# Kernel tuning notes

Measured on AMD Instinct MI355X. Metric: run time of the kernel, lower is better.

The kernel has to match this reference:

```python
import jax, jax.numpy as jnp
import numpy as np

B, N = 512, 4
OBS, OBSU, ID = 128, 64, 16
STATE = OBS + OBSU - ID  # 176
M1, M2, G1, A = 256, 256, 256, 16
E = 128  # hypernet_embed


def setup_inputs() -> dict:
    key = jax.random.key(0)
    ks = jax.random.split(key, 24)

    def W(k, shape):
        return jax.random.normal(k, shape, dtype=jnp.float32) * 0.05

    inp = {"input": jax.random.normal(ks[0], (B, N, OBS + OBSU), dtype=jnp.float32)}
    # layer1_hypernet: Linear(ID, 10*E)
    inp["l1_W"] = W(ks[1], (10 * E, ID)); inp["l1_b"] = W(ks[2], (10 * E,))
    # hyper_net{i}_w / hyper_net{i}_b : Linear(E, in*out) / Linear(E, out)
    inp["w1W"] = W(ks[3], (STATE * M1, E)); inp["w1b"] = W(ks[4], (STATE * M1,))
    inp["b1W"] = W(ks[5], (M1, E));        inp["b1b"] = W(ks[6], (M1,))
    inp["w2W"] = W(ks[7], (M1 * M2, E));   inp["w2b"] = W(ks[8], (M1 * M2,))
    inp["b2W"] = W(ks[9], (M2, E));        inp["b2b"] = W(ks[10], (M2,))
    inp["w3W"] = W(ks[11], (M2 * M2, E));  inp["w3b"] = W(ks[12], (M2 * M2,))
    inp["b3W"] = W(ks[13], (M2, E));       inp["b3b"] = W(ks[14], (M2,))
    inp["w4W"] = W(ks[15], (M2 * G1, E));  inp["w4b"] = W(ks[16], (M2 * G1,))
    inp["b4W"] = W(ks[17], (G1, E));       inp["b4b"] = W(ks[18], (G1,))
    inp["w5W"] = W(ks[19], (G1 * A, E));   inp["w5b"] = W(ks[20], (G1 * A,))
    inp["b5W"] = W(ks[21], (A, E));        inp["b5b"] = W(ks[22], (A,))
    return inp


def reference(input, l1_W, l1_b, w1W, w1b, b1W, b1b, w2W, w2b, b2W, b2b,
              w3W, w3b, b3W, b3b, w4W, w4b, b4W, b4b, w5W, w5b, b5W, b5b):
    b, n, d = input.shape
    BN = b * n
    ids = input[..., -ID:].reshape(BN, ID)
    x = input[..., :-ID].reshape(BN, d - ID)  # [BN, STATE]
    # layer1_hypernet: ReLU(Linear(ID -> 10E))
    h = jax.nn.relu(ids @ l1_W.T + l1_b)  # [BN, 10E]
    chunk = lambda i: h[:, i * E:(i + 1) * E]

    def layer(x, iw, ib, wW, wb, bW, bb, out_dim, act):
        # generate per-sample weight [BN, in, out] and bias [BN, out]
        Wm = (chunk(iw) @ wW.T + wb).reshape(BN, x.shape[-1], out_dim)
        bm = chunk(ib) @ bW.T + bb
        y = jnp.einsum('bs,bsm->bm', x, Wm) + bm  # batched GEMV
        return jax.nn.relu(y) if act else y

    out = layer(x,   0, 1, w1W, w1b, b1W, b1b, M1, True)
    out = layer(out, 2, 3, w2W, w2b, b2W, b2b, M2, True)
    out = layer(out, 4, 5, w3W, w3b, b3W, b3b, M2, True)
    out = layer(out, 6, 7, w4W, w4b, b4W, b4b, G1, False)  # no ReLU after layer 4
    out = layer(out, 8, 9, w5W, w5b, b5W, b5b, A, True)
    return out.reshape(b, n, A)
```

## Files before the change

kernel.cpp:

```cpp
#include <hip/hip_runtime.h>
#include <hip/hip_bf16.h>

#define E_ 128
#define NSAMP 2048

typedef __attribute__((ext_vector_type(8))) short short8;
typedef __attribute__((ext_vector_type(4))) float floatx4;

__device__ __forceinline__ ushort f2b(float f) {
    union { __hip_bfloat16 h; ushort u; } cv;
    cv.h = __float2bfloat16(f);
    return cv.u;
}

__device__ __forceinline__ void gload_lds16(const ushort* g, ushort* l) {
    __builtin_amdgcn_global_load_lds(
        (const __attribute__((address_space(1))) void*)g,
        (__attribute__((address_space(3))) void*)l, 16, 0, 0);
}

__global__ void hyper_h(const float* __restrict__ input, const float* __restrict__ l1W,
                        const float* __restrict__ l1b, float* __restrict__ h)
{
    int b = blockIdx.x / 5;
    int o = (blockIdx.x % 5) * 256 + threadIdx.x;
    const float* ids = input + (size_t)b * 192 + 176;
    const float* w = l1W + (size_t)o * 16;
    float a = l1b[o];
#pragma unroll
    for (int i = 0; i < 16; i += 4) {
        float4 wv = *(const float4*)(w + i);
        a += ids[i] * wv.x + ids[i + 1] * wv.y + ids[i + 2] * wv.z + ids[i + 3] * wv.w;
    }
    h[(size_t)b * 1280 + o] = fmaxf(a, 0.f);
}

__global__ void x0_t(const float* __restrict__ input, float* __restrict__ xT0)
{
    int idx = blockIdx.x * 256 + threadIdx.x;
    int s = idx >> 11, b = idx & 2047;
    xT0[idx] = input[(size_t)b * 192 + s];
}

__global__ void cvt_bf16(const float* __restrict__ src, ushort* __restrict__ dst, int n)
{
    int i = (blockIdx.x * 256 + threadIdx.x) * 8;
    if (i >= n) return;
    float4 a = *(const float4*)(src + i);
    float4 b = *(const float4*)(src + i + 4);
    union { ushort o[8]; uint4 v; } u;
    u.o[0] = f2b(a.x); u.o[1] = f2b(a.y); u.o[2] = f2b(a.z); u.o[3] = f2b(a.w);
    u.o[4] = f2b(b.x); u.o[5] = f2b(b.y); u.o[6] = f2b(b.z); u.o[7] = f2b(b.w);
    *(uint4*)(dst + i) = u.v;
}

__global__ void cvt_bias(const float* __restrict__ bW, const float* __restrict__ wb,
                         ushort* __restrict__ dst, int S, int M)
{
    int idx = blockIdx.x * 256 + threadIdx.x;
    int slice = idx / (M * E_);
    int rem = idx - slice * (M * E_);
    int m = rem / E_, e = rem - m * E_;
    ushort v;
    if (slice == 0) {
        v = f2b(bW[(size_t)m * E_ + e]);
    } else {
        int s = (slice - 1) * 128 + e;
        v = (s < S) ? f2b(wb[(size_t)s * M + m]) : (ushort)0;
    }
    dst[(size_t)(S + slice) * M * E_ + rem] = v;
}

__global__ __launch_bounds__(256, 2) void gemm_big(
    const ushort* __restrict__ wWb, const float* __restrict__ h,
    const float* __restrict__ xT, float* __restrict__ partial,
    int S, int iw, int ksplit, int btiles, int ntiles)
{
    __shared__ ushort As[128 * 64];
    __shared__ ushort Bs[128 * 64];

    const int tid = threadIdx.x;
    const int bt = blockIdx.x % btiles;
    const int nt = (blockIdx.x / btiles) % ntiles;
    const int ks = blockIdx.x / (btiles * ntiles);
    const int b0 = bt * 128;
    const int m0 = nt * 128;
    const int total_s = S + 3;
    const int base = total_s / ksplit;
    const int rem = total_s - base * ksplit;
    const int s0 = ks * base + min(ks, rem);
    const int s1 = s0 + base + (ks < rem ? 1 : 0);

    const int lane = tid & 63;
    const int wave = tid >> 6;
    const int quad = lane >> 4;
    const int lr = lane & 15;
    const int wm0 = (wave >> 1) * 64;
    const int wn0 = (wave & 1) * 64;

    const int tb = tid >> 3;
    const int teg = tid & 7;
    const int aswz = (teg ^ (tb & 7)) * 8;

    const int brow = lane >> 3;
    const int bgg = (lane & 7) ^ brow;

    float hreg[4][2][8];
#pragma unroll
    for (int k2 = 0; k2 < 4; ++k2) {
#pragma unroll
        for (int p = 0; p < 2; ++p) {
            const float* src = h + (size_t)(b0 + tb + 32 * k2) * 1280 + (size_t)iw * E_ + p * 64 + teg * 8;
            float4 v0 = *(const float4*)(src);
            float4 v1 = *(const float4*)(src + 4);
            hreg[k2][p][0] = v0.x; hreg[k2][p][1] = v0.y; hreg[k2][p][2] = v0.z; hreg[k2][p][3] = v0.w;
            hreg[k2][p][4] = v1.x; hreg[k2][p][5] = v1.y; hreg[k2][p][6] = v1.z; hreg[k2][p][7] = v1.w;
        }
    }

    floatx4 acc[4][4];
#pragma unroll
    for (int i = 0; i < 4; ++i)
#pragma unroll
        for (int j = 0; j < 4; ++j)
            acc[i][j] = (floatx4){0.f, 0.f, 0.f, 0.f};

    for (int s = s0; s < s1; ++s) {
        float xv[4];
        if (s < S) {
#pragma unroll
            for (int k2 = 0; k2 < 4; ++k2)
                xv[k2] = xT[(size_t)s * NSAMP + b0 + tb + 32 * k2];
        }

#pragma unroll
        for (int p = 0; p < 2; ++p) {
            __syncthreads();

#pragma unroll
            for (int t = 0; t < 4; ++t) {
                int rloc = wave * 32 + t * 8;
                const ushort* gp = wWb + ((size_t)s * 256 + m0 + rloc + brow) * E_ + p * 64 + bgg * 8;
                ushort* lp = &Bs[(size_t)rloc * 64] + lane * 8;
                gload_lds16(gp, lp);
            }

            if (s < S) {
#pragma unroll
                for (int k2 = 0; k2 < 4; ++k2) {
                    union { ushort o[8]; uint4 v; } u;
#pragma unroll
                    for (int j = 0; j < 8; ++j) u.o[j] = f2b(xv[k2] * hreg[k2][p][j]);
                    *(uint4*)&As[(size_t)(tb + 32 * k2) * 64 + aswz] = u.v;
                }
            } else if (s == S) {
#pragma unroll
                for (int k2 = 0; k2 < 4; ++k2) {
                    const float* src = h + (size_t)(b0 + tb + 32 * k2) * 1280
                                         + (size_t)(iw + 1) * E_ + p * 64 + teg * 8;
                    float4 v0 = *(const float4*)(src);
                    float4 v1 = *(const float4*)(src + 4);
                    union { ushort o[8]; uint4 v; } u;
                    u.o[0] = f2b(v0.x); u.o[1] = f2b(v0.y); u.o[2] = f2b(v0.z); u.o[3] = f2b(v0.w);
                    u.o[4] = f2b(v1.x); u.o[5] = f2b(v1.y); u.o[6] = f2b(v1.z); u.o[7] = f2b(v1.w);
                    *(uint4*)&As[(size_t)(tb + 32 * k2) * 64 + aswz] = u.v;
                }
            } else {
                int j0 = (s - S - 1) * 128 + p * 64 + teg * 8;
#pragma unroll
                for (int k2 = 0; k2 < 4; ++k2) {
                    int b = b0 + tb + 32 * k2;
                    union { ushort o[8]; uint4 v; } u;
#pragma unroll
                    for (int jj = 0; jj < 8; ++jj) {
                        int sp = j0 + jj;
                        u.o[jj] = (sp < S) ? f2b(xT[(size_t)sp * NSAMP + b]) : (ushort)0;
                    }
                    *(uint4*)&As[(size_t)(tb + 32 * k2) * 64 + aswz] = u.v;
                }
            }

            __syncthreads();

#pragma unroll
            for (int kk = 0; kk < 2; ++kk) {
                const int swz = ((kk * 4 + quad) ^ (lr & 7)) * 8;
                short8 af[4], bfr[4];
#pragma unroll
                for (int i = 0; i < 4; ++i)
                    af[i] = *(const short8*)&As[(size_t)(wm0 + i * 16 + lr) * 64 + swz];
#pragma unroll
                for (int j = 0; j < 4; ++j)
                    bfr[j] = *(const short8*)&Bs[(size_t)(wn0 + j * 16 + lr) * 64 + swz];
#pragma unroll
                for (int i = 0; i < 4; ++i)
#pragma unroll
                    for (int j = 0; j < 4; ++j)
                        acc[i][j] = __builtin_amdgcn_mfma_f32_16x16x32_bf16(af[i], bfr[j], acc[i][j], 0, 0, 0);
            }
        }
    }

    float* dst = partial + (size_t)ks * NSAMP * 256;
#pragma unroll
    for (int i = 0; i < 4; ++i)
#pragma unroll
        for (int j = 0; j < 4; ++j)
#pragma unroll
            for (int r = 0; r < 4; ++r) {
                int row = wm0 + i * 16 + quad * 4 + r;
                int col = wn0 + j * 16 + lr;
                dst[(size_t)(b0 + row) * 256 + m0 + col] = acc[i][j][r];
            }
}

template<int BM, int BN, int WROWS, int WCOLS>
__global__ __launch_bounds__(256, 2) void gemm_k(
    const ushort* __restrict__ wWb, const float* __restrict__ h,
    const float* __restrict__ xT, float* __restrict__ partial,
    int S, int M, int iw, int ksplit, int btiles, int ntiles)
{
    constexpr int SM = BM / WROWS / 16;
    constexpr int SN = BN / WCOLS / 16;
    constexpr int ASLOTS = BM * 8 / 256;
    constexpr int LDA = 72;

    __shared__ ushort As[BM][LDA];
    __shared__ ushort Bs[BN][LDA];

    const int tid = threadIdx.x;
    const int bt = blockIdx.x % btiles;
    const int nt = (blockIdx.x / btiles) % ntiles;
    const int ks = blockIdx.x / (btiles * ntiles);
    const int b0 = bt * BM;
    const int m0 = nt * BN;
    const int total_s = S + 3;
    const int base = total_s / ksplit;
    const int rem = total_s - base * ksplit;
    const int s0 = ks * base + min(ks, rem);
    const int s1 = s0 + base + (ks < rem ? 1 : 0);

    const int lane = tid & 63;
    const int wave = tid >> 6;
    const int quad = lane >> 4;
    const int lr = lane & 15;
    const int wm0 = (wave / WCOLS) * (BM / WROWS);
    const int wn0 = (wave % WCOLS) * (BN / WCOLS);

    const int tb = tid >> 3;
    const int teg = tid & 7;

    float hreg[ASLOTS][2][8];
#pragma unroll
    for (int k2 = 0; k2 < ASLOTS; ++k2) {
        int b = tb + 32 * k2;
#pragma unroll
        for (int p = 0; p < 2; ++p) {
            const float* src = h + (size_t)(b0 + b) * 1280 + (size_t)iw * E_ + p * 64 + teg * 8;
            float4 v0 = *(const float4*)(src);
            float4 v1 = *(const float4*)(src + 4);
            hreg[k2][p][0] = v0.x; hreg[k2][p][1] = v0.y; hreg[k2][p][2] = v0.z; hreg[k2][p][3] = v0.w;
            hreg[k2][p][4] = v1.x; hreg[k2][p][5] = v1.y; hreg[k2][p][6] = v1.z; hreg[k2][p][7] = v1.w;
        }
    }

    floatx4 acc[SM][SN];
#pragma unroll
    for (int i = 0; i < SM; ++i)
#pragma unroll
        for (int j = 0; j < SN; ++j)
            acc[i][j] = (floatx4){0.f, 0.f, 0.f, 0.f};

    for (int s = s0; s < s1; ++s) {
        float xv[ASLOTS];
        if (s < S) {
#pragma unroll
            for (int k2 = 0; k2 < ASLOTS; ++k2)
                xv[k2] = xT[(size_t)s * NSAMP + b0 + tb + 32 * k2];
        }

#pragma unroll
        for (int p = 0; p < 2; ++p) {
            if (s < S) {
#pragma unroll
                for (int k2 = 0; k2 < ASLOTS; ++k2) {
                    union { ushort o[8]; uint4 v; } u;
#pragma unroll
                    for (int j = 0; j < 8; ++j) u.o[j] = f2b(xv[k2] * hreg[k2][p][j]);
                    *(uint4*)&As[tb + 32 * k2][teg * 8] = u.v;
                }
            } else if (s == S) {
#pragma unroll
                for (int k2 = 0; k2 < ASLOTS; ++k2) {
                    const float* src = h + (size_t)(b0 + tb + 32 * k2) * 1280
                                         + (size_t)(iw + 1) * E_ + p * 64 + teg * 8;
                    float4 v0 = *(const float4*)(src);
                    float4 v1 = *(const float4*)(src + 4);
                    union { ushort o[8]; uint4 v; } u;
                    u.o[0] = f2b(v0.x); u.o[1] = f2b(v0.y); u.o[2] = f2b(v0.z); u.o[3] = f2b(v0.w);
                    u.o[4] = f2b(v1.x); u.o[5] = f2b(v1.y); u.o[6] = f2b(v1.z); u.o[7] = f2b(v1.w);
                    *(uint4*)&As[tb + 32 * k2][teg * 8] = u.v;
                }
            } else {
                int j0 = (s - S - 1) * 128 + p * 64 + teg * 8;
#pragma unroll
                for (int k2 = 0; k2 < ASLOTS; ++k2) {
                    int b = b0 + tb + 32 * k2;
                    union { ushort o[8]; uint4 v; } u;
#pragma unroll
                    for (int jj = 0; jj < 8; ++jj) {
                        int sp = j0 + jj;
                        u.o[jj] = (sp < S) ? f2b(xT[(size_t)sp * NSAMP + b]) : (ushort)0;
                    }
                    *(uint4*)&As[tb + 32 * k2][teg * 8] = u.v;
                }
            }
#pragma unroll
            for (int slot = tid; slot < BN * 8; slot += 256) {
                int m = slot >> 3, eg2 = slot & 7;
                *(uint4*)&Bs[m][eg2 * 8] =
                    *(const uint4*)(wWb + ((size_t)s * M + m0 + m) * E_ + p * 64 + eg2 * 8);
            }
            __syncthreads();
#pragma unroll
            for (int kk = 0; kk < 2; ++kk) {
                short8 af[SM], bfr[SN];
#pragma unroll
                for (int i = 0; i < SM; ++i)
                    af[i] = *(const short8*)&As[wm0 + i * 16 + lr][kk * 32 + quad * 8];
#pragma unroll
                for (int j = 0; j < SN; ++j)
                    bfr[j] = *(const short8*)&Bs[wn0 + j * 16 + lr][kk * 32 + quad * 8];
#pragma unroll
                for (int i = 0; i < SM; ++i)
#pragma unroll
                    for (int j = 0; j < SN; ++j)
                        acc[i][j] = __builtin_amdgcn_mfma_f32_16x16x32_bf16(af[i], bfr[j], acc[i][j], 0, 0, 0);
            }
            __syncthreads();
        }
    }

    float* dst = partial + (size_t)ks * NSAMP * M;
#pragma unroll
    for (int i = 0; i < SM; ++i)
#pragma unroll
        for (int j = 0; j < SN; ++j)
#pragma unroll
            for (int r = 0; r < 4; ++r) {
                int row = wm0 + i * 16 + quad * 4 + r;
                int col = wn0 + j * 16 + lr;
                dst[(size_t)(b0 + row) * M + m0 + col] = acc[i][j][r];
            }
}

__global__ void reduce_mid(const float* __restrict__ partial, const float* __restrict__ bb,
                           float* __restrict__ xTn, int KS, int relu)
{
    __shared__ float t[32][33];
    const int b0 = (blockIdx.x >> 3) * 32;
    const int m0 = (blockIdx.x & 7) * 32;
    const int mo = threadIdx.x & 31;
    const int bs0 = threadIdx.x >> 5;
    const float bv = bb[m0 + mo];
#pragma unroll
    for (int r = 0; r < 4; ++r) {
        const int bs = bs0 + 8 * r;
        const size_t off = (size_t)(b0 + bs) * 256 + m0 + mo;
        float a0 = 0.f, a1 = 0.f, a2 = 0.f, a3 = 0.f;
#pragma unroll
        for (int k = 0; k < 16; k += 4) {
            a0 += partial[(size_t)(k + 0) * (NSAMP * 256) + off];
            a1 += partial[(size_t)(k + 1) * (NSAMP * 256) + off];
            a2 += partial[(size_t)(k + 2) * (NSAMP * 256) + off];
            a3 += partial[(size_t)(k + 3) * (NSAMP * 256) + off];
        }
        float a = (a0 + a1) + (a2 + a3) + bv;
        if (relu) a = fmaxf(a, 0.f);
        t[bs][mo] = a;
    }
    __syncthreads();
    const int bo = threadIdx.x & 31;
    const int ms0 = threadIdx.x >> 5;
#pragma unroll
    for (int r = 0; r < 4; ++r) {
        const int ms = ms0 + 8 * r;
        xTn[(size_t)(m0 + ms) * NSAMP + b0 + bo] = t[bo][ms];
    }
}

__global__ void reduce_out(const float* __restrict__ partial, const float* __restrict__ bb,
                           float* __restrict__ out, int KS)
{
    int idx = blockIdx.x * 256 + threadIdx.x;
    float a0 = 0.f, a1 = 0.f, a2 = 0.f, a3 = 0.f;
#pragma unroll
    for (int k = 0; k < 32; k += 4) {
        a0 += partial[(size_t)(k + 0) * (NSAMP * 16) + idx];
        a1 += partial[(size_t)(k + 1) * (NSAMP * 16) + idx];
        a2 += partial[(size_t)(k + 2) * (NSAMP * 16) + idx];
        a3 += partial[(size_t)(k + 3) * (NSAMP * 16) + idx];
    }
    out[idx] = fmaxf((a0 + a1) + (a2 + a3) + bb[idx & 15], 0.f);
}

extern "C" void kernel_launch(void* const* d_in, const int* in_sizes, int n_in,
                              void* d_out, int out_size, void* d_ws, size_t ws_size,
                              hipStream_t stream)
{
    const float* input = (const float*)d_in[0];
    const float* l1W   = (const float*)d_in[1];
    const float* l1b   = (const float*)d_in[2];

    char* ws = (char*)d_ws;
    ushort* wWb = (ushort*)(ws + 0);
    float* h    = (float*)(ws + 16975872);
    float* xT0  = (float*)(ws + 27461632);
    float* xT1  = (float*)(ws + 29558784);
    float* part = (float*)(ws + 31655936);

    hipLaunchKernelGGL(hyper_h, dim3(2048 * 5), dim3(256), 0, stream, input, l1W, l1b, h);
    hipLaunchKernelGGL(x0_t, dim3(176 * 2048 / 256), dim3(256), 0, stream, input, xT0);

    const int S_[5] = {176, 256, 256, 256, 256};
    const int M_[5] = {256, 256, 256, 256, 16};
    float* xt[2] = {xT0, xT1};

    for (int i = 0; i < 5; ++i) {
        const float* wW = (const float*)d_in[3 + 4 * i];
        const float* wb = (const float*)d_in[4 + 4 * i];
        const float* bW = (const float*)d_in[5 + 4 * i];
        const float* bb = (const float*)d_in[6 + 4 * i];
        float* xin = xt[i & 1];
        int n = S_[i] * M_[i] * E_;
        hipLaunchKernelGGL(cvt_bf16, dim3(n / 2048), dim3(256), 0, stream, wW, wWb, n);
        hipLaunchKernelGGL(cvt_bias, dim3(3 * M_[i] * E_ / 256), dim3(256), 0, stream,
                           bW, wb, wWb, S_[i], M_[i]);

        if (M_[i] == 256) {
            const int btiles = 16, ntiles = 2, ksplit = 16;
            hipLaunchKernelGGL(gemm_big, dim3(btiles * ntiles * ksplit), dim3(256), 0, stream,
                               wWb, h, xin, part, S_[i], 2 * i, ksplit, btiles, ntiles);
            hipLaunchKernelGGL(reduce_mid, dim3(512), dim3(256), 0, stream,
                               part, bb, xt[(i + 1) & 1], ksplit, (i < 3) ? 1 : 0);
        } else {
            const int btiles = 8, ntiles = 1, ksplit = 32;
            hipLaunchKernelGGL((gemm_k<256, 16, 4, 1>), dim3(btiles * ntiles * ksplit), dim3(256), 0, stream,
                               wWb, h, xin, part, S_[i], 16, 2 * i, ksplit, btiles, ntiles);
            hipLaunchKernelGGL(reduce_out, dim3(128), dim3(256), 0, stream,
                               part, bb, (float*)d_out, ksplit);
        }
    }
}
```

Baseline: 580.3 us.

## Double-buffer LDS tiles in gemm_big to overlap weight DMA with MFMA

Splits the A and B shared-memory tiles into two buffers and restructures the loop into a software pipeline. The next phase's weight tile is DMA'd into the alternate buffer and its A tile generated there while the current phase's MFMAs run, cutting the two barriers per phase to one. This doubles LDS use to 64 KB per block, which may limit the two-blocks-per-CU occupancy target and raise register pressure.

```diff
diff --git a/kernel.cpp b/kernel.cpp
--- a/kernel.cpp
+++ b/kernel.cpp
@@ -76,8 +76,8 @@
     const float* __restrict__ xT, float* __restrict__ partial,
     int S, int iw, int ksplit, int btiles, int ntiles)
 {
-    __shared__ ushort As[128 * 64];
-    __shared__ ushort Bs[128 * 64];
+    __shared__ ushort As[2][128 * 64];
+    __shared__ ushort Bs[2][128 * 64];
 
     const int tid = threadIdx.x;
     const int bt = blockIdx.x % btiles;
@@ -125,79 +125,106 @@
         for (int j = 0; j < 4; ++j)
             acc[i][j] = (floatx4){0.f, 0.f, 0.f, 0.f};
 
-    for (int s = s0; s < s1; ++s) {
-        float xv[4];
+    float xv[4];
+
+    auto dma_B = [&](int s, int p, int buf) {
+#pragma unroll
+        for (int t = 0; t < 4; ++t) {
+            int rloc = wave * 32 + t * 8;
+            const ushort* gp = wWb + ((size_t)s * 256 + m0 + rloc + brow) * E_ + p * 64 + bgg * 8;
+            gload_lds16(gp, &Bs[buf][rloc * 64 + lane * 8]);
+        }
+    };
+
+    auto gen_A = [&](int s, int p, int buf) {
         if (s < S) {
 #pragma unroll
+            for (int k2 = 0; k2 < 4; ++k2) {
+                union { ushort o[8]; uint4 v; } u;
+#pragma unroll
+                for (int j = 0; j < 8; ++j) u.o[j] = f2b(xv[k2] * hreg[k2][p][j]);
+                *(uint4*)&As[buf][(tb + 32 * k2) * 64 + aswz] = u.v;
+            }
+        } else if (s == S) {
+#pragma unroll
+            for (int k2 = 0; k2 < 4; ++k2) {
+                const float* src = h + (size_t)(b0 + tb + 32 * k2) * 1280
+                                     + (size_t)(iw + 1) * E_ + p * 64 + teg * 8;
+                float4 v0 = *(const float4*)(src);
+                float4 v1 = *(const float4*)(src + 4);
+                union { ushort o[8]; uint4 v; } u;
+                u.o[0] = f2b(v0.x); u.o[1] = f2b(v0.y); u.o[2] = f2b(v0.z); u.o[3] = f2b(v0.w);
+                u.o[4] = f2b(v1.x); u.o[5] = f2b(v1.y); u.o[6] = f2b(v1.z); u.o[7] = f2b(v1.w);
+                *(uint4*)&As[buf][(tb + 32 * k2) * 64 + aswz] = u.v;
+            }
+        } else {
+            int j0 = (s - S - 1) * 128 + p * 64 + teg * 8;
+#pragma unroll
+            for (int k2 = 0; k2 < 4; ++k2) {
+                int b = b0 + tb + 32 * k2;
+                union { ushort o[8]; uint4 v; } u;
+#pragma unroll
+                for (int jj = 0; jj < 8; ++jj) {
+                    int sp = j0 + jj;
+                    u.o[jj] = (sp < S) ? f2b(xT[(size_t)sp * NSAMP + b]) : (ushort)0;
+                }
+                *(uint4*)&As[buf][(tb + 32 * k2) * 64 + aswz] = u.v;
+            }
+        }
+    };
+
+    const int nph = (s1 - s0) * 2;
+
+    if (s0 < S) {
+#pragma unroll
+        for (int k2 = 0; k2 < 4; ++k2)
+            xv[k2] = xT[(size_t)s0 * NSAMP + b0 + tb + 32 * k2];
+    }
+    dma_B(s0, 0, 0);
+    gen_A(s0, 0, 0);
+
+    for (int ph = 0; ph < nph; ++ph) {
+        const int cur = ph & 1;
+        const int np = ph + 1;
+        const int sn = s0 + (np >> 1);
+        const int pn = np & 1;
+        const bool stage = np < nph;
+
+        __syncthreads();
+
+        if (stage) dma_B(sn, pn, cur ^ 1);
+
+        float xvn[4];
+        const bool newx = stage && pn == 0 && sn < S;
+        if (newx) {
+#pragma unroll
             for (int k2 = 0; k2 < 4; ++k2)
-                xv[k2] = xT[(size_t)s * NSAMP + b0 + tb + 32 * k2];
-        }
-
-#pragma unroll
-        for (int p = 0; p < 2; ++p) {
-            __syncthreads();
-
-#pragma unroll
-            for (int t = 0; t < 4; ++t) {
-                int rloc = wave * 32 + t * 8;
-                const ushort* gp = wWb + ((size_t)s * 256 + m0 + rloc + brow) * E_ + p * 64 + bgg * 8;
-                ushort* lp = &Bs[(size_t)rloc * 64] + lane * 8;
-                gload_lds16(gp, lp);
-            }
-
-            if (s < S) {
-#pragma unroll
-                for (int k2 = 0; k2 < 4; ++k2) {
-                    union { ushort o[8]; uint4 v; } u;
-#pragma unroll
-                    for (int j = 0; j < 8; ++j) u.o[j] = f2b(xv[k2] * hreg[k2][p][j]);
-                    *(uint4*)&As[(size_t)(tb + 32 * k2) * 64 + aswz] = u.v;
-                }
-            } else if (s == S) {
-#pragma unroll
-                for (int k2 = 0; k2 < 4; ++k2) {
-                    const float* src = h + (size_t)(b0 + tb + 32 * k2) * 1280
-                                         + (size_t)(iw + 1) * E_ + p * 64 + teg * 8;
-                    float4 v0 = *(const float4*)(src);
-                    float4 v1 = *(const float4*)(src + 4);
-                    union { ushort o[8]; uint4 v; } u;
-                    u.o[0] = f2b(v0.x); u.o[1] = f2b(v0.y); u.o[2] = f2b(v0.z); u.o[3] = f2b(v0.w);
-                    u.o[4] = f2b(v1.x); u.o[5] = f2b(v1.y); u.o[6] = f2b(v1.z); u.o[7] = f2b(v1.w);
-                    *(uint4*)&As[(size_t)(tb + 32 * k2) * 64 + aswz] = u.v;
-                }
-            } else {
-                int j0 = (s - S - 1) * 128 + p * 64 + teg * 8;
-#pragma unroll
-                for (int k2 = 0; k2 < 4; ++k2) {
-                    int b = b0 + tb + 32 * k2;
-                    union { ushort o[8]; uint4 v; } u;
-#pragma unroll
-                    for (int jj = 0; jj < 8; ++jj) {
-                        int sp = j0 + jj;
-                        u.o[jj] = (sp < S) ? f2b(xT[(size_t)sp * NSAMP + b]) : (ushort)0;
-                    }
-                    *(uint4*)&As[(size_t)(tb + 32 * k2) * 64 + aswz] = u.v;
-                }
-            }
-
-            __syncthreads();
-
-#pragma unroll
-            for (int kk = 0; kk < 2; ++kk) {
-                const int swz = ((kk * 4 + quad) ^ (lr & 7)) * 8;
-                short8 af[4], bfr[4];
-#pragma unroll
-                for (int i = 0; i < 4; ++i)
-                    af[i] = *(const short8*)&As[(size_t)(wm0 + i * 16 + lr) * 64 + swz];
+                xvn[k2] = xT[(size_t)sn * NSAMP + b0 + tb + 32 * k2];
+        }
+
+#pragma unroll
+        for (int kk = 0; kk < 2; ++kk) {
+            const int swz = ((kk * 4 + quad) ^ (lr & 7)) * 8;
+            short8 af[4], bfr[4];
+#pragma unroll
+            for (int i = 0; i < 4; ++i)
+                af[i] = *(const short8*)&As[cur][(wm0 + i * 16 + lr) * 64 + swz];
+#pragma unroll
+            for (int j = 0; j < 4; ++j)
+                bfr[j] = *(const short8*)&Bs[cur][(wn0 + j * 16 + lr) * 64 + swz];
+#pragma unroll
+            for (int i = 0; i < 4; ++i)
 #pragma unroll
                 for (int j = 0; j < 4; ++j)
-                    bfr[j] = *(const short8*)&Bs[(size_t)(wn0 + j * 16 + lr) * 64 + swz];
-#pragma unroll
-                for (int i = 0; i < 4; ++i)
-#pragma unroll
-                    for (int j = 0; j < 4; ++j)
-                        acc[i][j] = __builtin_amdgcn_mfma_f32_16x16x32_bf16(af[i], bfr[j], acc[i][j], 0, 0, 0);
-            }
+                    acc[i][j] = __builtin_amdgcn_mfma_f32_16x16x32_bf16(af[i], bfr[j], acc[i][j], 0, 0, 0);
+        }
+
+        if (stage) {
+            if (newx) {
+#pragma unroll
+                for (int k2 = 0; k2 < 4; ++k2) xv[k2] = xvn[k2];
+            }
+            gen_A(sn, pn, cur ^ 1);
         }
     }
 
```

New measurement: 791.0 us. 36.3% more time.

## Restructure hypernet GEMM to factor x out of per-s MFMA and double-buffer weights

Applied to the files above, without the earlier changes.

The large-layer GEMM no longer builds an x*h product tile in LDS for each state index. It keeps bf16 h fragments in registers, computes W_s·h per s with MFMA, and scales the result by x[s] in fp32 before accumulating. Full 128x128 weight slices are double-buffered in LDS so the next slice loads while the current one is computed. The partial-output layout is transposed to [m][b], which lets reduce_mid become a plain vectorized sum with no LDS transpose. The risk is extra fp32 FMA work per s, higher register pressure, and more LDS use (64KB) that may lower occupancy.

```diff
diff --git a/kernel.cpp b/kernel.cpp
--- a/kernel.cpp
+++ b/kernel.cpp
@@ -71,50 +71,57 @@
     dst[(size_t)(S + slice) * M * E_ + rem] = v;
 }
 
-__global__ __launch_bounds__(256, 2) void gemm_big(
+__global__ __launch_bounds__(256, 2) void gemm_big2(
     const ushort* __restrict__ wWb, const float* __restrict__ h,
     const float* __restrict__ xT, float* __restrict__ partial,
-    int S, int iw, int ksplit, int btiles, int ntiles)
-{
-    __shared__ ushort As[128 * 64];
-    __shared__ ushort Bs[128 * 64];
+    int S, int iw, int ksplit)
+{
+    __shared__ ushort Ws[2][128 * 128];
 
     const int tid = threadIdx.x;
-    const int bt = blockIdx.x % btiles;
-    const int nt = (blockIdx.x / btiles) % ntiles;
-    const int ks = blockIdx.x / (btiles * ntiles);
+    const int mt = blockIdx.x & 1;
+    const int bt = (blockIdx.x >> 1) & 15;
+    const int ks = blockIdx.x >> 5;
+    const int m0 = mt * 128;
     const int b0 = bt * 128;
-    const int m0 = nt * 128;
     const int total_s = S + 3;
     const int base = total_s / ksplit;
     const int rem = total_s - base * ksplit;
     const int s0 = ks * base + min(ks, rem);
     const int s1 = s0 + base + (ks < rem ? 1 : 0);
+    const int sm = min(s1, S);
 
     const int lane = tid & 63;
     const int wave = tid >> 6;
     const int quad = lane >> 4;
     const int lr = lane & 15;
-    const int wm0 = (wave >> 1) * 64;
-    const int wn0 = (wave & 1) * 64;
-
-    const int tb = tid >> 3;
-    const int teg = tid & 7;
-    const int aswz = (teg ^ (tb & 7)) * 8;
-
-    const int brow = lane >> 3;
-    const int bgg = (lane & 7) ^ brow;
-
-    float hreg[4][2][8];
-#pragma unroll
-    for (int k2 = 0; k2 < 4; ++k2) {
-#pragma unroll
-        for (int p = 0; p < 2; ++p) {
-            const float* src = h + (size_t)(b0 + tb + 32 * k2) * 1280 + (size_t)iw * E_ + p * 64 + teg * 8;
-            float4 v0 = *(const float4*)(src);
-            float4 v1 = *(const float4*)(src + 4);
-            hreg[k2][p][0] = v0.x; hreg[k2][p][1] = v0.y; hreg[k2][p][2] = v0.z; hreg[k2][p][3] = v0.w;
-            hreg[k2][p][4] = v1.x; hreg[k2][p][5] = v1.y; hreg[k2][p][6] = v1.z; hreg[k2][p][7] = v1.w;
+    const int wm = (wave >> 1) * 64;
+    const int wb_ = (wave & 1) * 64;
+
+    const int dr = lane >> 4;
+    const int dg = lane & 15;
+
+#pragma unroll
+    for (int t = 0; t < 8; ++t) {
+        int rbase = (wave * 8 + t) * 4;
+        int r = rbase + dr;
+        int g = (dg & 8) | ((dg & 7) ^ (r & 7));
+        gload_lds16(wWb + ((size_t)s0 * 256 + m0 + r) * 128 + g * 8,
+                    &Ws[0][rbase * 128 + lane * 8]);
+    }
+
+    short8 hf[4][4];
+#pragma unroll
+    for (int j = 0; j < 4; ++j) {
+        const float* hr = h + (size_t)(b0 + wb_ + j * 16 + lr) * 1280 + (size_t)iw * E_;
+#pragma unroll
+        for (int kk = 0; kk < 4; ++kk) {
+            float4 v0 = *(const float4*)(hr + kk * 32 + quad * 8);
+            float4 v1 = *(const float4*)(hr + kk * 32 + quad * 8 + 4);
+            union { ushort o[8]; short8 v; } u;
+            u.o[0] = f2b(v0.x); u.o[1] = f2b(v0.y); u.o[2] = f2b(v0.z); u.o[3] = f2b(v0.w);
+            u.o[4] = f2b(v1.x); u.o[5] = f2b(v1.y); u.o[6] = f2b(v1.z); u.o[7] = f2b(v1.w);
+            hf[j][kk] = u.v;
         }
     }
 
@@ -125,92 +132,132 @@
         for (int j = 0; j < 4; ++j)
             acc[i][j] = (floatx4){0.f, 0.f, 0.f, 0.f};
 
-    for (int s = s0; s < s1; ++s) {
+    const floatx4 zf = (floatx4){0.f, 0.f, 0.f, 0.f};
+
+    int cur = 0;
+    for (int s = s0; s < sm; ++s) {
         float xv[4];
-        if (s < S) {
-#pragma unroll
-            for (int k2 = 0; k2 < 4; ++k2)
-                xv[k2] = xT[(size_t)s * NSAMP + b0 + tb + 32 * k2];
-        }
-
-#pragma unroll
-        for (int p = 0; p < 2; ++p) {
-            __syncthreads();
-
-#pragma unroll
-            for (int t = 0; t < 4; ++t) {
-                int rloc = wave * 32 + t * 8;
-                const ushort* gp = wWb + ((size_t)s * 256 + m0 + rloc + brow) * E_ + p * 64 + bgg * 8;
-                ushort* lp = &Bs[(size_t)rloc * 64] + lane * 8;
-                gload_lds16(gp, lp);
-            }
-
-            if (s < S) {
-#pragma unroll
-                for (int k2 = 0; k2 < 4; ++k2) {
-                    union { ushort o[8]; uint4 v; } u;
-#pragma unroll
-                    for (int j = 0; j < 8; ++j) u.o[j] = f2b(xv[k2] * hreg[k2][p][j]);
-                    *(uint4*)&As[(size_t)(tb + 32 * k2) * 64 + aswz] = u.v;
-                }
-            } else if (s == S) {
-#pragma unroll
-                for (int k2 = 0; k2 < 4; ++k2) {
-                    const float* src = h + (size_t)(b0 + tb + 32 * k2) * 1280
-                                         + (size_t)(iw + 1) * E_ + p * 64 + teg * 8;
-                    float4 v0 = *(const float4*)(src);
-                    float4 v1 = *(const float4*)(src + 4);
-                    union { ushort o[8]; uint4 v; } u;
+#pragma unroll
+        for (int j = 0; j < 4; ++j)
+            xv[j] = xT[(size_t)s * NSAMP + b0 + wb_ + j * 16 + lr];
+
+        __syncthreads();
+
+        if (s + 1 < sm) {
+#pragma unroll
+            for (int t = 0; t < 8; ++t) {
+                int rbase = (wave * 8 + t) * 4;
+                int r = rbase + dr;
+                int g = (dg & 8) | ((dg & 7) ^ (r & 7));
+                gload_lds16(wWb + ((size_t)(s + 1) * 256 + m0 + r) * 128 + g * 8,
+                            &Ws[cur ^ 1][rbase * 128 + lane * 8]);
+            }
+        }
+
+#pragma unroll
+        for (int i = 0; i < 4; ++i) {
+            const int r = wm + i * 16 + lr;
+            short8 af[4];
+#pragma unroll
+            for (int kk = 0; kk < 4; ++kk) {
+                int g = kk * 4 + quad;
+                int g2 = (g & 8) | ((g & 7) ^ (r & 7));
+                af[kk] = *(const short8*)&Ws[cur][r * 128 + g2 * 8];
+            }
+            floatx4 Gj[4];
+#pragma unroll
+            for (int j = 0; j < 4; ++j)
+                Gj[j] = __builtin_amdgcn_mfma_f32_16x16x32_bf16(af[0], hf[j][0], zf, 0, 0, 0);
+#pragma unroll
+            for (int kk = 1; kk < 4; ++kk)
+#pragma unroll
+                for (int j = 0; j < 4; ++j)
+                    Gj[j] = __builtin_amdgcn_mfma_f32_16x16x32_bf16(af[kk], hf[j][kk], Gj[j], 0, 0, 0);
+#pragma unroll
+            for (int j = 0; j < 4; ++j)
+                acc[i][j] += xv[j] * Gj[j];
+        }
+        cur ^= 1;
+    }
+
+    for (int s = sm; s < s1; ++s) {
+        __syncthreads();
+#pragma unroll
+        for (int t = 0; t < 8; ++t) {
+            int rbase = (wave * 8 + t) * 4;
+            int r = rbase + dr;
+            int g = (dg & 8) | ((dg & 7) ^ (r & 7));
+            gload_lds16(wWb + ((size_t)s * 256 + m0 + r) * 128 + g * 8,
+                        &Ws[0][rbase * 128 + lane * 8]);
+        }
+        short8 bfb[4][4];
+        if (s == S) {
+#pragma unroll
+            for (int j = 0; j < 4; ++j) {
+                const float* hr = h + (size_t)(b0 + wb_ + j * 16 + lr) * 1280 + (size_t)(iw + 1) * E_;
+#pragma unroll
+                for (int kk = 0; kk < 4; ++kk) {
+                    float4 v0 = *(const float4*)(hr + kk * 32 + quad * 8);
+                    float4 v1 = *(const float4*)(hr + kk * 32 + quad * 8 + 4);
+                    union { ushort o[8]; short8 v; } u;
                     u.o[0] = f2b(v0.x); u.o[1] = f2b(v0.y); u.o[2] = f2b(v0.z); u.o[3] = f2b(v0.w);
                     u.o[4] = f2b(v1.x); u.o[5] = f2b(v1.y); u.o[6] = f2b(v1.z); u.o[7] = f2b(v1.w);
-                    *(uint4*)&As[(size_t)(tb + 32 * k2) * 64 + aswz] = u.v;
+                    bfb[j][kk] = u.v;
                 }
-            } else {
-                int j0 = (s - S - 1) * 128 + p * 64 + teg * 8;
-#pragma unroll
-                for (int k2 = 0; k2 < 4; ++k2) {
-                    int b = b0 + tb + 32 * k2;
-                    union { ushort o[8]; uint4 v; } u;
-#pragma unroll
-                    for (int jj = 0; jj < 8; ++jj) {
-                        int sp = j0 + jj;
-                        u.o[jj] = (sp < S) ? f2b(xT[(size_t)sp * NSAMP + b]) : (ushort)0;
+            }
+        } else {
+            int off = (s - S - 1) * 128;
+#pragma unroll
+            for (int j = 0; j < 4; ++j) {
+                int b = b0 + wb_ + j * 16 + lr;
+#pragma unroll
+                for (int kk = 0; kk < 4; ++kk) {
+                    union { ushort o[8]; short8 v; } u;
+#pragma unroll
+                    for (int t = 0; t < 8; ++t) {
+                        int sp = off + kk * 32 + quad * 8 + t;
+                        u.o[t] = (sp < S) ? f2b(xT[(size_t)sp * NSAMP + b]) : (ushort)0;
                     }
-                    *(uint4*)&As[(size_t)(tb + 32 * k2) * 64 + aswz] = u.v;
+                    bfb[j][kk] = u.v;
                 }
             }
-
-            __syncthreads();
-
-#pragma unroll
-            for (int kk = 0; kk < 2; ++kk) {
-                const int swz = ((kk * 4 + quad) ^ (lr & 7)) * 8;
-                short8 af[4], bfr[4];
-#pragma unroll
-                for (int i = 0; i < 4; ++i)
-                    af[i] = *(const short8*)&As[(size_t)(wm0 + i * 16 + lr) * 64 + swz];
+        }
+        __syncthreads();
+#pragma unroll
+        for (int i = 0; i < 4; ++i) {
+            const int r = wm + i * 16 + lr;
+            short8 af[4];
+#pragma unroll
+            for (int kk = 0; kk < 4; ++kk) {
+                int g = kk * 4 + quad;
+                int g2 = (g & 8) | ((g & 7) ^ (r & 7));
+                af[kk] = *(const short8*)&Ws[0][r * 128 + g2 * 8];
+            }
+            floatx4 Gj[4];
+#pragma unroll
+            for (int j = 0; j < 4; ++j)
+                Gj[j] = __builtin_amdgcn_mfma_f32_16x16x32_bf16(af[0], bfb[j][0], zf, 0, 0, 0);
+#pragma unroll
+            for (int kk = 1; kk < 4; ++kk)
 #pragma unroll
                 for (int j = 0; j < 4; ++j)
-                    bfr[j] = *(const short8*)&Bs[(size_t)(wn0 + j * 16 + lr) * 64 + swz];
-#pragma unroll
-                for (int i = 0; i < 4; ++i)
-#pragma unroll
-                    for (int j = 0; j < 4; ++j)
-                        acc[i][j] = __builtin_amdgcn_mfma_f32_16x16x32_bf16(af[i], bfr[j], acc[i][j], 0, 0, 0);
-            }
-        }
-    }
-
-    float* dst = partial + (size_t)ks * NSAMP * 256;
+                    Gj[j] = __builtin_amdgcn_mfma_f32_16x16x32_bf16(af[kk], bfb[j][kk], Gj[j], 0, 0, 0);
+#pragma unroll
+            for (int j = 0; j < 4; ++j)
+                acc[i][j] += Gj[j];
+        }
+    }
+
+    float* dst = partial + (size_t)ks * (256 * NSAMP);
 #pragma unroll
     for (int i = 0; i < 4; ++i)
 #pragma unroll
         for (int j = 0; j < 4; ++j)
 #pragma unroll
             for (int r = 0; r < 4; ++r) {
-                int row = wm0 + i * 16 + quad * 4 + r;
-                int col = wn0 + j * 16 + lr;
-                dst[(size_t)(b0 + row) * 256 + m0 + col] = acc[i][j][r];
+                int m = m0 + wm + i * 16 + quad * 4 + r;
+                int b = b0 + wb_ + j * 16 + lr;
+                dst[(size_t)m * NSAMP + b] = acc[i][j][r];
             }
 }
 
@@ -357,36 +404,22 @@
 __global__ void reduce_mid(const float* __restrict__ partial, const float* __restrict__ bb,
                            float* __restrict__ xTn, int KS, int relu)
 {
-    __shared__ float t[32][33];
-    const int b0 = (blockIdx.x >> 3) * 32;
-    const int m0 = (blockIdx.x & 7) * 32;
-    const int mo = threadIdx.x & 31;
-    const int bs0 = threadIdx.x >> 5;
-    const float bv = bb[m0 + mo];
-#pragma unroll
-    for (int r = 0; r < 4; ++r) {
-        const int bs = bs0 + 8 * r;
-        const size_t off = (size_t)(b0 + bs) * 256 + m0 + mo;
-        float a0 = 0.f, a1 = 0.f, a2 = 0.f, a3 = 0.f;
-#pragma unroll
-        for (int k = 0; k < 16; k += 4) {
-            a0 += partial[(size_t)(k + 0) * (NSAMP * 256) + off];
-            a1 += partial[(size_t)(k + 1) * (NSAMP * 256) + off];
-            a2 += partial[(size_t)(k + 2) * (NSAMP * 256) + off];
-            a3 += partial[(size_t)(k + 3) * (NSAMP * 256) + off];
-        }
-        float a = (a0 + a1) + (a2 + a3) + bv;
-        if (relu) a = fmaxf(a, 0.f);
-        t[bs][mo] = a;
-    }
-    __syncthreads();
-    const int bo = threadIdx.x & 31;
-    const int ms0 = threadIdx.x >> 5;
-#pragma unroll
-    for (int r = 0; r < 4; ++r) {
-        const int ms = ms0 + 8 * r;
-        xTn[(size_t)(m0 + ms) * NSAMP + b0 + bo] = t[bo][ms];
-    }
+    int idx = (blockIdx.x * 256 + threadIdx.x) * 4;
+    int m = idx >> 11;
+    floatx4 a0 = {0.f,0.f,0.f,0.f}, a1 = a0, a2 = a0, a3 = a0;
+#pragma unroll 4
+    for (int k = 0; k < KS; k += 4) {
+        a0 += *(const floatx4*)&partial[(size_t)(k + 0) * (256 * NSAMP) + idx];
+        a1 += *(const floatx4*)&partial[(size_t)(k + 1) * (256 * NSAMP) + idx];
+        a2 += *(const floatx4*)&partial[(size_t)(k + 2) * (256 * NSAMP) + idx];
+        a3 += *(const floatx4*)&partial[(size_t)(k + 3) * (256 * NSAMP) + idx];
+    }
+    floatx4 r = (a0 + a1) + (a2 + a3) + bb[m];
+    if (relu) {
+        r[0] = fmaxf(r[0], 0.f); r[1] = fmaxf(r[1], 0.f);
+        r[2] = fmaxf(r[2], 0.f); r[3] = fmaxf(r[3], 0.f);
+    }
+    *(floatx4*)&xTn[idx] = r;
 }
 
 __global__ void reduce_out(const float* __restrict__ partial, const float* __restrict__ bb,
@@ -438,11 +471,10 @@
                            bW, wb, wWb, S_[i], M_[i]);
 
         if (M_[i] == 256) {
-            const int btiles = 16, ntiles = 2, ksplit = 16;
-            hipLaunchKernelGGL(gemm_big, dim3(btiles * ntiles * ksplit), dim3(256), 0, stream,
-                               wWb, h, xin, part, S_[i], 2 * i, ksplit, btiles, ntiles);
+            hipLaunchKernelGGL(gemm_big2, dim3(512), dim3(256), 0, stream,
+                               wWb, h, xin, part, S_[i], 2 * i, 16);
             hipLaunchKernelGGL(reduce_mid, dim3(512), dim3(256), 0, stream,
-                               part, bb, xt[(i + 1) & 1], ksplit, (i < 3) ? 1 : 0);
+                               part, bb, xt[(i + 1) & 1], 16, (i < 3) ? 1 : 0);
         } else {
             const int btiles = 8, ntiles = 1, ksplit = 32;
             hipLaunchKernelGGL((gemm_k<256, 16, 4, 1>), dim3(btiles * ntiles * ksplit), dim3(256), 0, stream,
```

Measured after the change: 637.0 us. +9.8%, slower.
